# Kernel tuning notes

Measured on AMD Instinct MI355X. Metric: run time of the kernel, lower is better.

Reference implementation:

```python
import jax, jax.numpy as jnp
import numpy as np

VOCAB = 50257   # N_max = len(word_to_idx)
IN_DIM = 256
HID = 13        # forced: out Linear in_features = 2*hidden_dim must equal dec output 2*13
L = 2048


def _lstm_dir(seq, Wih, Whh, b, reverse):
    """Single-direction LSTM over seq [T, F] with zero init. b = b_ih + b_hh.
    Torch gate order: i, f, g, o."""
    H = Whh.shape[1]

    def step(carry, x_t):
        h, c = carry
        z = Wih @ x_t + Whh @ h + b                  # (4H,)
        i, f, g, o = jnp.split(z, 4)
        c2 = jax.nn.sigmoid(f) * c + jax.nn.sigmoid(i) * jnp.tanh(g)
        h2 = jax.nn.sigmoid(o) * jnp.tanh(c2)
        return (h2, c2), h2

    init = (jnp.zeros((H,), seq.dtype), jnp.zeros((H,), seq.dtype))
    (hn, cn), hs = jax.lax.scan(step, init, seq, reverse=reverse)
    return hs, hn, cn


def _dec_cell(x_scalar, h, c, Wih, Whh, b):
    """One LSTM cell step with scalar input (input_size=1). Returns new h."""
    z = Wih[:, 0] * x_scalar + Whh @ h + b
    i, f, g, o = jnp.split(z, 4)
    c2 = jax.nn.sigmoid(f) * c + jax.nn.sigmoid(i) * jnp.tanh(g)
    return jax.nn.sigmoid(o) * jnp.tanh(c2)


def setup_inputs() -> dict:
    key = jax.random.key(0)
    ks = jax.random.split(key, 16)
    s = 0.05
    G = 4 * HID  # 52; also num_layers*2*HID = 52 (proj in_features)
    return {
        "x": jax.random.randint(ks[0], (L,), 0, VOCAB),
        "emb_W": jax.random.normal(ks[1], (VOCAB + 1, IN_DIM)) * s,
        "enc_Wih0": jax.random.normal(ks[2], (2, G, IN_DIM)) * s,   # [dir, 4H, in]
        "enc_Whh0": jax.random.normal(ks[3], (2, G, HID)) * s,
        "enc_b0": jax.random.normal(ks[4], (2, G)) * s,
        "enc_Wih1": jax.random.normal(ks[5], (2, G, 2 * HID)) * s,  # layer1 input = 2*HID
        "enc_Whh1": jax.random.normal(ks[6], (2, G, HID)) * s,
        "enc_b1": jax.random.normal(ks[7], (2, G)) * s,
        "proj1_W": jax.random.normal(ks[8], (2 * HID, 2 * 2 * HID)) * s,
        "proj1_b": jax.random.normal(ks[9], (2 * HID,)) * s,
        "proj2_W": jax.random.normal(ks[10], (2 * HID, 2 * 2 * HID)) * s,
        "proj2_b": jax.random.normal(ks[11], (2 * HID,)) * s,
        "dec_Wih": jax.random.normal(ks[12], (2, G, 1)) * s,
        "dec_Whh": jax.random.normal(ks[13], (2, G, HID)) * s,
        "dec_b": jax.random.normal(ks[14], (2, G)) * s,
        "out_W": jax.random.normal(ks[15], (VOCAB, 2 * HID)) * s,
        "out_b": jnp.zeros((VOCAB,), jnp.float32),
    }


def reference(x, emb_W, enc_Wih0, enc_Whh0, enc_b0, enc_Wih1, enc_Whh1, enc_b1,
              proj1_W, proj1_b, proj2_W, proj2_b, dec_Wih, dec_Whh, dec_b,
              out_W, out_b):
    embs = emb_W[x]                                            # (L, IN_DIM)

    # Encoder: 2-layer bidirectional LSTM, batch=1 (vectors).
    hs_f0, hnf0, cnf0 = _lstm_dir(embs, enc_Wih0[0], enc_Whh0[0], enc_b0[0], False)
    hs_b0, hnb0, cnb0 = _lstm_dir(embs, enc_Wih0[1], enc_Whh0[1], enc_b0[1], True)
    out0 = jnp.concatenate([hs_f0, hs_b0], axis=-1)            # (L, 2*HID)
    _, hnf1, cnf1 = _lstm_dir(out0, enc_Wih1[0], enc_Whh1[0], enc_b1[0], False)
    _, hnb1, cnb1 = _lstm_dir(out0, enc_Wih1[1], enc_Whh1[1], enc_b1[1], True)

    # torch h_n layout: [l0_fwd, l0_bwd, l1_fwd, l1_bwd]
    h_flat = jnp.concatenate([hnf0, hnb0, hnf1, hnb1])         # (52,)
    c_flat = jnp.concatenate([cnf0, cnb0, cnf1, cnb1])
    state_h = (proj1_W @ h_flat + proj1_b).reshape(2, HID)     # dec (dir, HID) init
    state_c = (proj2_W @ c_flat + proj2_b).reshape(2, HID)

    # Decoder step 0: input -1.0 with projected initial state.
    start = jnp.float32(-1.0)
    step0 = jnp.concatenate([
        _dec_cell(start, state_h[0], state_c[0], dec_Wih[0], dec_Whh[0], dec_b[0]),
        _dec_cell(start, state_h[1], state_c[1], dec_Wih[1], dec_Whh[1], dec_b[1]),
    ])                                                          # (26,)

    # Steps i>0: original code calls self.dec(input) with NO hidden state, so each
    # step uses zero initial state and depends only on x[i-1] -> fully parallel.
    xs = x[:-1].astype(jnp.float32)                             # (L-1,)
    z0 = jnp.zeros((HID,), jnp.float32)
    rest = jax.vmap(lambda v: jnp.concatenate([
        _dec_cell(v, z0, z0, dec_Wih[0], dec_Whh[0], dec_b[0]),
        _dec_cell(v, z0, z0, dec_Wih[1], dec_Whh[1], dec_b[1]),
    ]))(xs)                                                     # (L-1, 26)

    dec_out = jnp.concatenate([step0[None, :], rest], axis=0)   # (L, 26)
    preds = dec_out @ out_W.T + out_b                           # (L, VOCAB)
    return preds, embs
```

## Files before the change

kernel.cpp:

```cpp
#include <hip/hip_runtime.h>
#include <hip/hip_bf16.h>
#include <cstdint>
#include <cstddef>

#define L      2048
#define IN_DIM 256
#define HID    13
#define G      52
#define VOCAB  50257
#define PRED_N ((size_t)L * VOCAB)
#define L2E    1.4426950408889634f
#define INV2L2E 0.34657359027997264f
#define NTX    25
#define NTILE  (NTX * 16)
#define GB     254
#define DYNLDS 49152

static __device__ __forceinline__ float fexp2(float x) { return __builtin_amdgcn_exp2f(x); }
static __device__ __forceinline__ float frcp(float x) { return __builtin_amdgcn_rcpf(x); }
static __device__ __forceinline__ float sigm(float z) { return 1.f - frcp(fexp2(z * L2E) + 1.f); }
static __device__ __forceinline__ float tanh_(float z) { return 1.f - 2.f * frcp(fexp2(z * (2.f * L2E)) + 1.f); }
static __device__ __forceinline__ float bcast(float v, int l) {
    return __int_as_float(__builtin_amdgcn_readlane(__float_as_int(v), l));
}

__global__ void __launch_bounds__(160) k_emb_u0(
    const int* __restrict__ x, const float* __restrict__ embW,
    const float* __restrict__ Wih0, const float* __restrict__ b0,
    const float* __restrict__ dWih, const float* __restrict__ db,
    float* __restrict__ out_embs, float* __restrict__ u0, float* __restrict__ dec)
{
    __shared__ float se[IN_DIM];
    int t = blockIdx.x;
    int tid = threadIdx.x;
    if (tid < 128) {
        int rowx = x[t];
        float2 e = ((const float2*)(embW + (size_t)rowx * IN_DIM))[tid];
        se[2 * tid]     = e.x;
        se[2 * tid + 1] = e.y;
        ((float2*)(out_embs + (size_t)t * IN_DIM))[tid] = e;
    }
    __syncthreads();
    if (tid < 2 * G) {
        int dirg = tid / G, g = tid % G;
        int gate = g / HID, row = g % HID;
        float msc = (gate == 2) ? 2.f * L2E : L2E;
        float acc = b0[dirg * G + g];
        const float* w = Wih0 + (size_t)(dirg * G + g) * IN_DIM;
        #pragma unroll 8
        for (int k = 0; k < IN_DIM; ++k)
            acc = fmaf(w[k], se[k], acc);
        u0[((size_t)dirg * L + t) * 64 + gate * 16 + row] = msc * acc;
    } else if (tid < 128) {
        int p = tid - 2 * G;
        int dirp = p / 12, pp = p % 12;
        int gate = pp / 3, row = HID + pp % 3;
        u0[((size_t)dirp * L + t) * 64 + gate * 16 + row] = 0.f;
    } else if (tid < 128 + 2 * HID && t >= 1) {
        int j = tid - 128;
        int dir = j / HID, jj = j % HID;
        float v = (float)x[t - 1];
        int base = dir * G;
        float zi = fmaf(dWih[base + jj],           v, db[base + jj]);
        float zg = fmaf(dWih[base + 2 * HID + jj], v, db[base + 2 * HID + jj]);
        float zo = fmaf(dWih[base + 3 * HID + jj], v, db[base + 3 * HID + jj]);
        float c2 = sigm(zi) * tanh_(zg);
        dec[(size_t)t * (2 * HID) + j] = sigm(zo) * tanh_(c2);
    }
}

template<bool DOUT>
static __device__ __forceinline__ void compute8(
    const float* buf, const float* whh, float kcv, float onev,
    bool m16, bool m32, float& h, float& c, float* outp, int pstep)
{
    #pragma unroll
    for (int k = 0; k < 8; ++k) {
        float h0 = bcast(h, 0), h1 = bcast(h, 1), h2 = bcast(h, 2), h3 = bcast(h, 3);
        float h4 = bcast(h, 4), h5 = bcast(h, 5), h6 = bcast(h, 6), h7 = bcast(h, 7);
        float h8_ = bcast(h, 8), h9 = bcast(h, 9), h10 = bcast(h, 10), h11 = bcast(h, 11);
        float h12 = bcast(h, 12);
        float A = fmaf(whh[0], h0, buf[k]);
        float B = whh[1] * h1;
        float C = whh[2] * h2;
        float D = whh[3] * h3;
        A = fmaf(whh[4], h4, A);   B = fmaf(whh[5], h5, B);
        C = fmaf(whh[6], h6, C);   D = fmaf(whh[7], h7, D);
        A = fmaf(whh[8], h8_, A);  B = fmaf(whh[9], h9, B);
        C = fmaf(whh[10], h10, C); D = fmaf(whh[11], h11, D);
        A = fmaf(whh[12], h12, A);
        float z = (A + B) + (C + D);
        float act = fmaf(-kcv, frcp(fexp2(z) + 1.f), onev);
        float pa = act, pb = act;
        asm("s_nop 1\n\tv_permlane16_swap_b32 %0, %1" : "+v"(pa), "+v"(pb));
        float sf = m16 ? pa : pb;
        float qa = act, qb = act;
        asm("s_nop 1\n\tv_permlane32_swap_b32 %0, %1" : "+v"(qa), "+v"(qb));
        float tg = m32 ? qa : qb;
        float ra = tg, rb = tg;
        asm("s_nop 1\n\tv_permlane16_swap_b32 %0, %1" : "+v"(ra), "+v"(rb));
        float so = m16 ? ra : rb;
        float c2 = fmaf(sf, c, act * tg);
        float th = fmaf(-2.f, frcp(fexp2(c2) + 1.f), 1.f);
        h = so * th;
        c = c2;
        if (DOUT) outp[k * pstep] = h;
    }
}

template<bool DOUT>
static __device__ __forceinline__ void chain_core(
    const float* ub, int pstep, const float* whh, float kcv, float onev,
    bool m16, bool m32, float* outp, float& hout, float& cout)
{
    float bufA[8], bufB[8];
    float h = 0.f, c = 0.f;
    #pragma unroll
    for (int k = 0; k < 8; ++k) bufA[k] = ub[k * pstep];
    #pragma unroll
    for (int k = 0; k < 8; ++k) bufB[k] = ub[(8 + k) * pstep];

    for (int tcb = 0; tcb < L; tcb += 16) {
        compute8<DOUT>(bufA, whh, kcv, onev, m16, m32, h, c, outp, pstep);
        if (DOUT) outp += 8 * pstep;
        if (tcb + 16 < L) {
            #pragma unroll
            for (int k = 0; k < 8; ++k) bufA[k] = ub[(tcb + 16 + k) * pstep];
        }
        compute8<DOUT>(bufB, whh, kcv, onev, m16, m32, h, c, outp, pstep);
        if (DOUT) outp += 8 * pstep;
        if (tcb + 24 < L) {
            #pragma unroll
            for (int k = 0; k < 8; ++k) bufB[k] = ub[(tcb + 24 + k) * pstep];
        }
    }
    hout = h; cout = c;
}

template<bool DOUT>
static __device__ __forceinline__ void run_chain(
    const float* u, const float* Whh, float* out0p,
    float* finh, float* finc, int chain_base, int dir, int lane)
{
    int lg16 = lane & 15, gate = lane >> 4;
    int rsrc = gate * HID + (lg16 < HID ? lg16 : HID - 1);
    float kcv, onev;
    if (gate == 2)      { kcv = 2.f;        onev = 1.f; }
    else if (gate == 0) { kcv = 2.f * L2E;  onev = 2.f * L2E; }
    else                { kcv = 1.f;        onev = 1.f; }
    float msc = (gate == 2) ? 2.f * L2E : L2E;
    float whh[HID];
    #pragma unroll
    for (int k = 0; k < HID; ++k) whh[k] = msc * Whh[(dir * G + rsrc) * HID + k];

    int ia = lane, ib = lane;
    asm("s_nop 1\n\tv_permlane16_swap_b32 %0, %1" : "+v"(ia), "+v"(ib));
    bool m16 = (ia == (lane ^ 16));
    int ja = lane, jb = lane;
    asm("s_nop 1\n\tv_permlane32_swap_b32 %0, %1" : "+v"(ja), "+v"(jb));
    bool m32 = (ja == (lane ^ 32));

    const float* ub = u + (size_t)dir * L * 64 + (dir ? (size_t)(L - 1) * 64 : 0) + lane;
    int pstep = dir ? -64 : 64;
    float* outp = out0p ? out0p + ((size_t)dir * L + (dir ? L - 1 : 0)) * 64 + lane : (float*)nullptr;

    float h, c;
    chain_core<DOUT>(ub, pstep, whh, kcv, onev, m16, m32, outp, h, c);

    if (lane < HID) {
        finh[(chain_base + dir) * HID + lane] = h;
        finc[(chain_base + dir) * HID + lane] = c * INV2L2E;
    }
}

__global__ void __launch_bounds__(1024) k_phase0(
    const float* __restrict__ u, const float* __restrict__ Whh,
    float* __restrict__ out0p, float* __restrict__ finh, float* __restrict__ finc,
    const float* __restrict__ dec, const float* __restrict__ outW,
    const float* __restrict__ outb, float* __restrict__ preds)
{
    extern __shared__ float sd[];
    int bid = blockIdx.x;
    int tid = threadIdx.x;
    if (bid < 2) {
        if (tid >= 64) return;
        __builtin_amdgcn_s_setprio(3);
        run_chain<true>(u, Whh, out0p, finh, finc, 0, bid, tid);
        return;
    }
    __builtin_amdgcn_s_setprio(0);
    int b = bid - 2;
    const int q = NTILE / GB, r = NTILE % GB;
    int start = b * q + (b < r ? b : r);
    int cnt   = q + (b < r ? 1 : 0);
    for (int tt = 0; tt < cnt; ++tt) {
        int tile = start + tt;
        int ix = tile % NTX, iy = tile / NTX;
        int nbase = ix * 2048, i0 = iy * 128;
        __syncthreads();
        for (int li = tid; li < 128 * 26; li += 1024) {
            int rr = li / 26, cc = li % 26;
            sd[rr * 28 + cc] = dec[(size_t)(i0 + rr) * 26 + cc];
        }
        __syncthreads();
        int n0 = nbase + tid, n1 = nbase + 1024 + tid;
        bool a0 = n0 < VOCAB, a1 = n1 < VOCAB;
        float w0[26], w1[26], b0v = 0.f, b1v = 0.f;
        #pragma unroll
        for (int k = 0; k < 26; ++k) { w0[k] = 0.f; w1[k] = 0.f; }
        if (a0) { const float* w = outW + (size_t)n0 * 26;
            #pragma unroll
            for (int k = 0; k < 26; ++k) w0[k] = w[k];
            b0v = outb[n0]; }
        if (a1) { const float* w = outW + (size_t)n1 * 26;
            #pragma unroll
            for (int k = 0; k < 26; ++k) w1[k] = w[k];
            b1v = outb[n1]; }
        for (int i = 0; i < 128; ++i) {
            int grow = i0 + i;
            float acc0 = b0v, acc1 = b1v;
            const float* dr = sd + i * 28;
            #pragma unroll
            for (int k = 0; k < 26; ++k) {
                float d = dr[k];
                acc0 = fmaf(d, w0[k], acc0);
                acc1 = fmaf(d, w1[k], acc1);
            }
            if (grow != 0) {
                size_t rb = (size_t)grow * VOCAB;
                if (a0) preds[rb + n0] = acc0;
                if (a1) preds[rb + n1] = acc1;
            }
        }
    }
}

__global__ void k_u1(const float* __restrict__ out0p, const float* __restrict__ Wih1,
                     const float* __restrict__ b1, float* __restrict__ u1)
{
    int idx = blockIdx.x * blockDim.x + threadIdx.x;
    if (idx >= L * 2 * 64) return;
    int t    = idx >> 7;
    int remv = idx & 127;
    int d1   = remv >> 6;
    int lane = remv & 63;
    int gate = lane >> 4, row = lane & 15;
    size_t oidx = ((size_t)d1 * L + t) * 64 + lane;
    if (row >= HID) { u1[oidx] = 0.f; return; }
    int g = gate * HID + row;
    float msc = (gate == 2) ? 2.f * L2E : L2E;
    float acc = b1[d1 * G + g];
    const float* w = Wih1 + (size_t)(d1 * G + g) * (2 * HID);
    const float* o0 = out0p + (size_t)t * 64;
    const float* o1 = out0p + ((size_t)L + t) * 64;
    #pragma unroll
    for (int k = 0; k < HID; ++k)
        acc = fmaf(w[k], o0[k], acc);
    #pragma unroll
    for (int k = 0; k < HID; ++k)
        acc = fmaf(w[HID + k], o1[k], acc);
    u1[oidx] = msc * acc;
}

__global__ void __launch_bounds__(64) k_phase1(
    const float* __restrict__ u, const float* __restrict__ Whh,
    float* __restrict__ finh, float* __restrict__ finc)
{
    run_chain<false>(u, Whh, (float*)nullptr, finh, finc, 2, blockIdx.x, threadIdx.x);
}

__global__ void __launch_bounds__(64) k_final(const float* __restrict__ fin_h, const float* __restrict__ fin_c,
                                              const float* __restrict__ p1W, const float* __restrict__ p1b,
                                              const float* __restrict__ p2W, const float* __restrict__ p2b,
                                              const float* __restrict__ dWih, const float* __restrict__ dWhh,
                                              const float* __restrict__ db, float* __restrict__ dec)
{
    __shared__ float sh[2 * HID], sc[2 * HID], sz[G];
    int tid = threadIdx.x;
    if (tid < 4 * HID) {
        int r = tid < 2 * HID ? tid : tid - 2 * HID;
        const float* W   = tid < 2 * HID ? p1W : p2W;
        const float* src = tid < 2 * HID ? fin_h : fin_c;
        float acc = tid < 2 * HID ? p1b[r] : p2b[r];
        for (int k = 0; k < 4 * HID; ++k) acc = fmaf(W[r * 4 * HID + k], src[k], acc);
        if (tid < 2 * HID) sh[r] = acc; else sc[r] = acc;
    }
    __syncthreads();
    for (int dir = 0; dir < 2; ++dir) {
        if (tid < G) {
            float acc = db[dir * G + tid] - dWih[dir * G + tid];
            for (int k = 0; k < HID; ++k)
                acc = fmaf(dWhh[(dir * G + tid) * HID + k], sh[dir * HID + k], acc);
            sz[tid] = acc;
        }
        __syncthreads();
        if (tid < HID) {
            float si = sigm(sz[tid]);
            float sf = sigm(sz[HID + tid]);
            float tg = tanh_(sz[2 * HID + tid]);
            float so = sigm(sz[3 * HID + tid]);
            float c2 = fmaf(sf, sc[dir * HID + tid], si * tg);
            dec[dir * HID + tid] = so * tanh_(c2);
        }
        __syncthreads();
    }
}

__global__ void k_row0(const float* __restrict__ dec, const float* __restrict__ outW,
                       const float* __restrict__ outb, float* __restrict__ preds)
{
    int n = blockIdx.x * blockDim.x + threadIdx.x;
    if (n >= VOCAB) return;
    float acc = outb[n];
    const float* w = outW + (size_t)n * 26;
    #pragma unroll
    for (int k = 0; k < 26; ++k) acc = fmaf(w[k], dec[k], acc);
    preds[n] = acc;
}

extern "C" void kernel_launch(void* const* d_in, const int* in_sizes, int n_in,
                              void* d_out, int out_size, void* d_ws, size_t ws_size,
                              hipStream_t stream)
{
    (void)in_sizes; (void)n_in; (void)out_size; (void)ws_size;

    const int*   x     = (const int*)d_in[0];
    const float* embW  = (const float*)d_in[1];
    const float* eWih0 = (const float*)d_in[2];
    const float* eWhh0 = (const float*)d_in[3];
    const float* eb0   = (const float*)d_in[4];
    const float* eWih1 = (const float*)d_in[5];
    const float* eWhh1 = (const float*)d_in[6];
    const float* eb1   = (const float*)d_in[7];
    const float* p1W   = (const float*)d_in[8];
    const float* p1b   = (const float*)d_in[9];
    const float* p2W   = (const float*)d_in[10];
    const float* p2b   = (const float*)d_in[11];
    const float* dWih  = (const float*)d_in[12];
    const float* dWhh  = (const float*)d_in[13];
    const float* db    = (const float*)d_in[14];
    const float* outW  = (const float*)d_in[15];
    const float* outb  = (const float*)d_in[16];

    float* ws    = (float*)d_ws;
    float* u0    = ws;
    float* u1    = u0 + 2 * L * 64;
    float* out0p = u1 + 2 * L * 64;
    float* dec   = out0p + 2 * L * 64;
    float* fin_h = dec + L * 2 * HID;
    float* fin_c = fin_h + 64;

    float* preds    = (float*)d_out;
    float* out_embs = preds + PRED_N;

    hipLaunchKernelGGL(k_emb_u0, dim3(L), dim3(160), 0, stream,
                       x, embW, eWih0, eb0, dWih, db, out_embs, u0, dec);

    hipLaunchKernelGGL(k_phase0, dim3(2 + GB), dim3(1024), DYNLDS, stream,
                       u0, eWhh0, out0p, fin_h, fin_c,
                       dec, outW, outb, preds);

    hipLaunchKernelGGL(k_u1, dim3((L * 2 * 64 + 255) / 256), dim3(256), 0, stream,
                       out0p, eWih1, eb1, u1);

    hipLaunchKernelGGL(k_phase1, dim3(2), dim3(64), 0, stream,
                       u1, eWhh1, fin_h, fin_c);

    hipLaunchKernelGGL(k_final, dim3(1), dim3(64), 0, stream,
                       fin_h, fin_c, p1W, p1b, p2W, p2b, dWih, dWhh, db, dec);

    hipLaunchKernelGGL(k_row0, dim3((VOCAB + 255) / 256), dim3(256), 0, stream,
                       dec, outW, outb, preds);
}
```

Baseline: 616.2 us.

## Split output GEMM across both LSTM chain phases to overlap with layer-1 recurrence

The output projection GEMM was previously overlapped only with the layer-0 recurrent chain. It is now split into narrower tiles (1024 columns, 512 threads), with 400 tiles run alongside layer 0 and the remaining 400 alongside the layer-1 chain in k_phase1. The goal is to hide the serial layer-1 LSTM latency behind useful GEMM work instead of leaving most of the GPU idle. In exchange, weight reuse per tile drops with narrower blocks, the dec tile is reloaded more often, and the serial chains may contend with GEMM blocks for CU resources.

```diff
diff --git a/kernel.cpp b/kernel.cpp
--- a/kernel.cpp
+++ b/kernel.cpp
@@ -11,10 +11,10 @@
 #define PRED_N ((size_t)L * VOCAB)
 #define L2E    1.4426950408889634f
 #define INV2L2E 0.34657359027997264f
-#define NTX    25
+#define NTX    50
 #define NTILE  (NTX * 16)
+#define NT0    400
 #define GB     254
-#define DYNLDS 49152
 
 static __device__ __forceinline__ float fexp2(float x) { return __builtin_amdgcn_exp2f(x); }
 static __device__ __forceinline__ float frcp(float x) { return __builtin_amdgcn_rcpf(x); }
@@ -173,37 +173,25 @@
     }
 }
 
-__global__ void __launch_bounds__(1024) k_phase0(
-    const float* __restrict__ u, const float* __restrict__ Whh,
-    float* __restrict__ out0p, float* __restrict__ finh, float* __restrict__ finc,
+static __device__ __forceinline__ void gemm_tiles(
+    int b, int tid, int tbase, int tcnt,
     const float* __restrict__ dec, const float* __restrict__ outW,
-    const float* __restrict__ outb, float* __restrict__ preds)
-{
-    extern __shared__ float sd[];
-    int bid = blockIdx.x;
-    int tid = threadIdx.x;
-    if (bid < 2) {
-        if (tid >= 64) return;
-        __builtin_amdgcn_s_setprio(3);
-        run_chain<true>(u, Whh, out0p, finh, finc, 0, bid, tid);
-        return;
-    }
-    __builtin_amdgcn_s_setprio(0);
-    int b = bid - 2;
-    const int q = NTILE / GB, r = NTILE % GB;
-    int start = b * q + (b < r ? b : r);
+    const float* __restrict__ outb, float* __restrict__ preds, float* sd)
+{
+    const int q = tcnt / GB, r = tcnt % GB;
+    int start = tbase + b * q + (b < r ? b : r);
     int cnt   = q + (b < r ? 1 : 0);
     for (int tt = 0; tt < cnt; ++tt) {
         int tile = start + tt;
         int ix = tile % NTX, iy = tile / NTX;
-        int nbase = ix * 2048, i0 = iy * 128;
+        int nbase = ix * 1024, i0 = iy * 128;
         __syncthreads();
-        for (int li = tid; li < 128 * 26; li += 1024) {
+        for (int li = tid; li < 128 * 26; li += 512) {
             int rr = li / 26, cc = li % 26;
             sd[rr * 28 + cc] = dec[(size_t)(i0 + rr) * 26 + cc];
         }
         __syncthreads();
-        int n0 = nbase + tid, n1 = nbase + 1024 + tid;
+        int n0 = nbase + tid, n1 = nbase + 512 + tid;
         bool a0 = n0 < VOCAB, a1 = n1 < VOCAB;
         float w0[26], w1[26], b0v = 0.f, b1v = 0.f;
         #pragma unroll
@@ -233,6 +221,25 @@
             }
         }
     }
+}
+
+__global__ void __launch_bounds__(512) k_phase0(
+    const float* __restrict__ u, const float* __restrict__ Whh,
+    float* __restrict__ out0p, float* __restrict__ finh, float* __restrict__ finc,
+    const float* __restrict__ dec, const float* __restrict__ outW,
+    const float* __restrict__ outb, float* __restrict__ preds)
+{
+    __shared__ float sd[128 * 28];
+    int bid = blockIdx.x;
+    int tid = threadIdx.x;
+    if (bid < 2) {
+        if (tid >= 64) return;
+        __builtin_amdgcn_s_setprio(3);
+        run_chain<true>(u, Whh, out0p, finh, finc, 0, bid, tid);
+        return;
+    }
+    __builtin_amdgcn_s_setprio(0);
+    gemm_tiles(bid - 2, tid, 0, NT0, dec, outW, outb, preds, sd);
 }
 
 __global__ void k_u1(const float* __restrict__ out0p, const float* __restrict__ Wih1,
@@ -262,11 +269,23 @@
     u1[oidx] = msc * acc;
 }
 
-__global__ void __launch_bounds__(64) k_phase1(
+__global__ void __launch_bounds__(512) k_phase1(
     const float* __restrict__ u, const float* __restrict__ Whh,
-    float* __restrict__ finh, float* __restrict__ finc)
-{
-    run_chain<false>(u, Whh, (float*)nullptr, finh, finc, 2, blockIdx.x, threadIdx.x);
+    float* __restrict__ finh, float* __restrict__ finc,
+    const float* __restrict__ dec, const float* __restrict__ outW,
+    const float* __restrict__ outb, float* __restrict__ preds)
+{
+    __shared__ float sd[128 * 28];
+    int bid = blockIdx.x;
+    int tid = threadIdx.x;
+    if (bid < 2) {
+        if (tid >= 64) return;
+        __builtin_amdgcn_s_setprio(3);
+        run_chain<false>(u, Whh, (float*)nullptr, finh, finc, 2, bid, tid);
+        return;
+    }
+    __builtin_amdgcn_s_setprio(0);
+    gemm_tiles(bid - 2, tid, NT0, NTILE - NT0, dec, outW, outb, preds, sd);
 }
 
 __global__ void __launch_bounds__(64) k_final(const float* __restrict__ fin_h, const float* __restrict__ fin_c,
@@ -356,15 +375,16 @@
     hipLaunchKernelGGL(k_emb_u0, dim3(L), dim3(160), 0, stream,
                        x, embW, eWih0, eb0, dWih, db, out_embs, u0, dec);
 
-    hipLaunchKernelGGL(k_phase0, dim3(2 + GB), dim3(1024), DYNLDS, stream,
+    hipLaunchKernelGGL(k_phase0, dim3(2 + GB), dim3(512), 0, stream,
                        u0, eWhh0, out0p, fin_h, fin_c,
                        dec, outW, outb, preds);
 
     hipLaunchKernelGGL(k_u1, dim3((L * 2 * 64 + 255) / 256), dim3(256), 0, stream,
                        out0p, eWih1, eb1, u1);
 
-    hipLaunchKernelGGL(k_phase1, dim3(2), dim3(64), 0, stream,
-                       u1, eWhh1, fin_h, fin_c);
+    hipLaunchKernelGGL(k_phase1, dim3(2 + GB), dim3(512), 0, stream,
+                       u1, eWhh1, fin_h, fin_c,
+                       dec, outW, outb, preds);
 
     hipLaunchKernelGGL(k_final, dim3(1), dim3(64), 0, stream,
                        fin_h, fin_c, p1W, p1b, p2W, p2b, dWih, dWhh, db, dec);
```

After: 607.1 us. Within noise of the previous version (-1.5%).

## Interleave u buffers for vector loads, specialize chain masks, shrink GEMM tiles

Applied to the files above, without the earlier changes.

Stores the u0/u1 gate pre-activations so that four consecutive timesteps of one lane are contiguous, which lets the recurrent chain fetch its inputs with 16-byte vector loads instead of scalar strided loads. The permlane mask selections and the direction become template parameters resolved once through readlane, which removes per-step selects. The co-scheduled output GEMM blocks drop from 1024 to 256 threads with narrower vocab tiles (NTX 99) and static shared memory. The smaller blocks and more tiles change occupancy and tile overhead in the preds write, and the eight template instantiations grow code size.

```diff
diff --git a/kernel.cpp b/kernel.cpp
--- a/kernel.cpp
+++ b/kernel.cpp
@@ -11,10 +11,11 @@
 #define PRED_N ((size_t)L * VOCAB)
 #define L2E    1.4426950408889634f
 #define INV2L2E 0.34657359027997264f
-#define NTX    25
+#define NTX    99
 #define NTILE  (NTX * 16)
 #define GB     254
-#define DYNLDS 49152
+
+typedef float v4f __attribute__((ext_vector_type(4)));
 
 static __device__ __forceinline__ float fexp2(float x) { return __builtin_amdgcn_exp2f(x); }
 static __device__ __forceinline__ float frcp(float x) { return __builtin_amdgcn_rcpf(x); }
@@ -23,6 +24,8 @@
 static __device__ __forceinline__ float bcast(float v, int l) {
     return __int_as_float(__builtin_amdgcn_readlane(__float_as_int(v), l));
 }
+
+#define UIDX(dirv, t, l4) ((size_t)(dirv) * L * 64 + ((t) >> 2) * 256 + (l4) * 4 + ((t) & 3))
 
 __global__ void __launch_bounds__(160) k_emb_u0(
     const int* __restrict__ x, const float* __restrict__ embW,
@@ -50,12 +53,12 @@
         #pragma unroll 8
         for (int k = 0; k < IN_DIM; ++k)
             acc = fmaf(w[k], se[k], acc);
-        u0[((size_t)dirg * L + t) * 64 + gate * 16 + row] = msc * acc;
+        u0[UIDX(dirg, t, gate * 16 + row)] = msc * acc;
     } else if (tid < 128) {
         int p = tid - 2 * G;
         int dirp = p / 12, pp = p % 12;
-        int gate = pp / 3, row = HID + pp % 3;
-        u0[((size_t)dirp * L + t) * 64 + gate * 16 + row] = 0.f;
+        int g4 = (pp / 3) * 16 + HID + pp % 3;
+        u0[UIDX(dirp, t, g4)] = 0.f;
     } else if (tid < 128 + 2 * HID && t >= 1) {
         int j = tid - 128;
         int dir = j / HID, jj = j % HID;
@@ -69,18 +72,21 @@
     }
 }
 
-template<bool DOUT>
+template<bool DOUT, int DIR, bool M16, bool M32>
 static __device__ __forceinline__ void compute8(
-    const float* buf, const float* whh, float kcv, float onev,
-    bool m16, bool m32, float& h, float& c, float* outp, int pstep)
+    v4f af, v4f bf, const float* whh, float kcv, float onev,
+    float& h, float& c, float* outp, int pstep)
 {
     #pragma unroll
     for (int k = 0; k < 8; ++k) {
+        float uk;
+        if (DIR == 0) uk = (k < 4) ? af[k] : bf[k - 4];
+        else          uk = (k < 4) ? bf[3 - k] : af[7 - k];
         float h0 = bcast(h, 0), h1 = bcast(h, 1), h2 = bcast(h, 2), h3 = bcast(h, 3);
         float h4 = bcast(h, 4), h5 = bcast(h, 5), h6 = bcast(h, 6), h7 = bcast(h, 7);
         float h8_ = bcast(h, 8), h9 = bcast(h, 9), h10 = bcast(h, 10), h11 = bcast(h, 11);
         float h12 = bcast(h, 12);
-        float A = fmaf(whh[0], h0, buf[k]);
+        float A = fmaf(whh[0], h0, uk);
         float B = whh[1] * h1;
         float C = whh[2] * h2;
         float D = whh[3] * h3;
@@ -93,13 +99,13 @@
         float act = fmaf(-kcv, frcp(fexp2(z) + 1.f), onev);
         float pa = act, pb = act;
         asm("s_nop 1\n\tv_permlane16_swap_b32 %0, %1" : "+v"(pa), "+v"(pb));
-        float sf = m16 ? pa : pb;
+        float sf = M16 ? pa : pb;
         float qa = act, qb = act;
         asm("s_nop 1\n\tv_permlane32_swap_b32 %0, %1" : "+v"(qa), "+v"(qb));
-        float tg = m32 ? qa : qb;
+        float tg = M32 ? qa : qb;
         float ra = tg, rb = tg;
         asm("s_nop 1\n\tv_permlane16_swap_b32 %0, %1" : "+v"(ra), "+v"(rb));
-        float so = m16 ? ra : rb;
+        float so = M16 ? ra : rb;
         float c2 = fmaf(sf, c, act * tg);
         float th = fmaf(-2.f, frcp(fexp2(c2) + 1.f), 1.f);
         h = so * th;
@@ -108,32 +114,32 @@
     }
 }
 
-template<bool DOUT>
+template<bool DOUT, int DIR, bool M16, bool M32>
 static __device__ __forceinline__ void chain_core(
-    const float* ub, int pstep, const float* whh, float kcv, float onev,
-    bool m16, bool m32, float* outp, float& hout, float& cout)
-{
-    float bufA[8], bufB[8];
+    const float* ubase, const float* whh, float kcv, float onev,
+    float* outp, int pstep_out, float& hout, float& cout)
+{
+    #define QOFF(s) ((DIR == 0) ? (s) * 64 : (L - 8 - (s)) * 64)
+    v4f a0 = *(const v4f*)(ubase + QOFF(0));
+    v4f b0 = *(const v4f*)(ubase + QOFF(0) + 256);
+    v4f a1 = *(const v4f*)(ubase + QOFF(8));
+    v4f b1 = *(const v4f*)(ubase + QOFF(8) + 256);
     float h = 0.f, c = 0.f;
-    #pragma unroll
-    for (int k = 0; k < 8; ++k) bufA[k] = ub[k * pstep];
-    #pragma unroll
-    for (int k = 0; k < 8; ++k) bufB[k] = ub[(8 + k) * pstep];
-
     for (int tcb = 0; tcb < L; tcb += 16) {
-        compute8<DOUT>(bufA, whh, kcv, onev, m16, m32, h, c, outp, pstep);
-        if (DOUT) outp += 8 * pstep;
+        compute8<DOUT, DIR, M16, M32>(a0, b0, whh, kcv, onev, h, c, outp, pstep_out);
+        if (DOUT) outp += 8 * pstep_out;
         if (tcb + 16 < L) {
-            #pragma unroll
-            for (int k = 0; k < 8; ++k) bufA[k] = ub[(tcb + 16 + k) * pstep];
-        }
-        compute8<DOUT>(bufB, whh, kcv, onev, m16, m32, h, c, outp, pstep);
-        if (DOUT) outp += 8 * pstep;
+            a0 = *(const v4f*)(ubase + QOFF(tcb + 16));
+            b0 = *(const v4f*)(ubase + QOFF(tcb + 16) + 256);
+        }
+        compute8<DOUT, DIR, M16, M32>(a1, b1, whh, kcv, onev, h, c, outp, pstep_out);
+        if (DOUT) outp += 8 * pstep_out;
         if (tcb + 24 < L) {
-            #pragma unroll
-            for (int k = 0; k < 8; ++k) bufB[k] = ub[(tcb + 24 + k) * pstep];
-        }
-    }
+            a1 = *(const v4f*)(ubase + QOFF(tcb + 24));
+            b1 = *(const v4f*)(ubase + QOFF(tcb + 24) + 256);
+        }
+    }
+    #undef QOFF
     hout = h; cout = c;
 }
 
@@ -155,17 +161,27 @@
 
     int ia = lane, ib = lane;
     asm("s_nop 1\n\tv_permlane16_swap_b32 %0, %1" : "+v"(ia), "+v"(ib));
-    bool m16 = (ia == (lane ^ 16));
+    int m16i = __builtin_amdgcn_readlane((ia == (lane ^ 16)) ? 1 : 0, 0);
     int ja = lane, jb = lane;
     asm("s_nop 1\n\tv_permlane32_swap_b32 %0, %1" : "+v"(ja), "+v"(jb));
-    bool m32 = (ja == (lane ^ 32));
-
-    const float* ub = u + (size_t)dir * L * 64 + (dir ? (size_t)(L - 1) * 64 : 0) + lane;
-    int pstep = dir ? -64 : 64;
+    int m32i = __builtin_amdgcn_readlane((ja == (lane ^ 32)) ? 1 : 0, 0);
+
+    const float* ubase = u + (size_t)dir * L * 64 + lane * 4;
+    int pstep_out = dir ? -64 : 64;
     float* outp = out0p ? out0p + ((size_t)dir * L + (dir ? L - 1 : 0)) * 64 + lane : (float*)nullptr;
 
     float h, c;
-    chain_core<DOUT>(ub, pstep, whh, kcv, onev, m16, m32, outp, h, c);
+    if (dir == 0) {
+        if (m16i) { if (m32i) chain_core<DOUT,0,true, true >(ubase, whh, kcv, onev, outp, pstep_out, h, c);
+                    else      chain_core<DOUT,0,true, false>(ubase, whh, kcv, onev, outp, pstep_out, h, c); }
+        else      { if (m32i) chain_core<DOUT,0,false,true >(ubase, whh, kcv, onev, outp, pstep_out, h, c);
+                    else      chain_core<DOUT,0,false,false>(ubase, whh, kcv, onev, outp, pstep_out, h, c); }
+    } else {
+        if (m16i) { if (m32i) chain_core<DOUT,1,true, true >(ubase, whh, kcv, onev, outp, pstep_out, h, c);
+                    else      chain_core<DOUT,1,true, false>(ubase, whh, kcv, onev, outp, pstep_out, h, c); }
+        else      { if (m32i) chain_core<DOUT,1,false,true >(ubase, whh, kcv, onev, outp, pstep_out, h, c);
+                    else      chain_core<DOUT,1,false,false>(ubase, whh, kcv, onev, outp, pstep_out, h, c); }
+    }
 
     if (lane < HID) {
         finh[(chain_base + dir) * HID + lane] = h;
@@ -173,13 +189,13 @@
     }
 }
 
-__global__ void __launch_bounds__(1024) k_phase0(
+__global__ void __launch_bounds__(256) k_phase0(
     const float* __restrict__ u, const float* __restrict__ Whh,
     float* __restrict__ out0p, float* __restrict__ finh, float* __restrict__ finc,
     const float* __restrict__ dec, const float* __restrict__ outW,
     const float* __restrict__ outb, float* __restrict__ preds)
 {
-    extern __shared__ float sd[];
+    __shared__ float sd[128][28];
     int bid = blockIdx.x;
     int tid = threadIdx.x;
     if (bid < 2) {
@@ -196,14 +212,14 @@
     for (int tt = 0; tt < cnt; ++tt) {
         int tile = start + tt;
         int ix = tile % NTX, iy = tile / NTX;
-        int nbase = ix * 2048, i0 = iy * 128;
+        int nbase = ix * 512, i0 = iy * 128;
         __syncthreads();
-        for (int li = tid; li < 128 * 26; li += 1024) {
+        for (int li = tid; li < 128 * 26; li += 256) {
             int rr = li / 26, cc = li % 26;
-            sd[rr * 28 + cc] = dec[(size_t)(i0 + rr) * 26 + cc];
+            sd[rr][cc] = dec[(size_t)(i0 + rr) * 26 + cc];
         }
         __syncthreads();
-        int n0 = nbase + tid, n1 = nbase + 1024 + tid;
+        int n0 = nbase + tid, n1 = nbase + 256 + tid;
         bool a0 = n0 < VOCAB, a1 = n1 < VOCAB;
         float w0[26], w1[26], b0v = 0.f, b1v = 0.f;
         #pragma unroll
@@ -219,7 +235,7 @@
         for (int i = 0; i < 128; ++i) {
             int grow = i0 + i;
             float acc0 = b0v, acc1 = b1v;
-            const float* dr = sd + i * 28;
+            const float* dr = sd[i];
             #pragma unroll
             for (int k = 0; k < 26; ++k) {
                 float d = dr[k];
@@ -245,7 +261,7 @@
     int d1   = remv >> 6;
     int lane = remv & 63;
     int gate = lane >> 4, row = lane & 15;
-    size_t oidx = ((size_t)d1 * L + t) * 64 + lane;
+    size_t oidx = UIDX(d1, t, lane);
     if (row >= HID) { u1[oidx] = 0.f; return; }
     int g = gate * HID + row;
     float msc = (gate == 2) ? 2.f * L2E : L2E;
@@ -356,7 +372,7 @@
     hipLaunchKernelGGL(k_emb_u0, dim3(L), dim3(160), 0, stream,
                        x, embW, eWih0, eb0, dWih, db, out_embs, u0, dec);
 
-    hipLaunchKernelGGL(k_phase0, dim3(2 + GB), dim3(1024), DYNLDS, stream,
+    hipLaunchKernelGGL(k_phase0, dim3(2 + GB), dim3(256), 0, stream,
                        u0, eWhh0, out0p, fin_h, fin_c,
                        dec, outW, outb, preds);
 
```

Measured after the change: 570.1 us. 1.08x faster.
